# Performance work log

Measured on AMD Instinct MI355X. Metric: run time of the kernel, lower is better.

Reference implementation:

```python
import jax, jax.numpy as jnp
import numpy as np

VS = 0.4
SENT = np.int32(2_000_000_000)  # > max lin code (1000^3)
EPS = 1e-5


def setup_inputs() -> dict:
    key = jax.random.key(0)
    ks = jax.random.split(key, 16)
    B, N, Cin, Cout = 8, 65536, 16, 128
    xyz = jax.random.uniform(ks[0], (B, N, 3), jnp.float32) * 51.2  # 128^3 voxel grid @ 0.4m
    feat = jax.random.normal(ks[1], (B, N, Cin), jnp.float32)
    mask = (jax.random.uniform(ks[2], (B, N)) < 0.9).astype(jnp.float32)
    def conv_w(k, ci, co):
        return jax.random.normal(k, (27, ci, co), jnp.float32) * (1.0 / np.sqrt(27.0 * ci))
    return {
        'xyz': xyz, 'feat': feat, 'mask': mask,
        'W1': conv_w(ks[3], Cin, 32), 'b1': jnp.zeros((32,), jnp.float32),
        'g1': jnp.ones((32,), jnp.float32), 'be1': jnp.zeros((32,), jnp.float32),
        'W2': conv_w(ks[4], 32, 64), 'b2': jnp.zeros((64,), jnp.float32),
        'g2': jnp.ones((64,), jnp.float32), 'be2': jnp.zeros((64,), jnp.float32),
        'W3': conv_w(ks[5], 64, Cout), 'b3': jnp.zeros((Cout,), jnp.float32),
        'g3': jnp.ones((Cout,), jnp.float32), 'be3': jnp.zeros((Cout,), jnp.float32),
    }


def _voxelize(lin_b, f_b, m_b):
    # sort-based unique with inverse; fixed capacity N slots (sentinel-padded)
    N = lin_b.shape[0]
    order = jnp.argsort(lin_b)
    s = lin_b[order]
    isnew = jnp.concatenate([jnp.ones((1,), bool), s[1:] != s[:-1]])
    rank = (jnp.cumsum(isnew) - 1).astype(jnp.int32)
    inv = jnp.zeros_like(lin_b).at[order].set(rank)          # point -> voxel slot
    unq = jnp.full_like(lin_b, SENT).at[rank].set(s)         # sorted unique codes, sentinel fill
    fsum = jax.ops.segment_sum(f_b * m_b[:, None], inv, num_segments=N)
    cnt = jnp.clip(jax.ops.segment_sum(m_b, inv, num_segments=N), 1.0)
    return unq, inv, fsum / cnt[:, None]


def _subm_conv(vfeat, unq, valid, W, b):
    # submanifold 3x3x3 conv on active voxels; neighbor lookup via binary search in sorted codes
    B, N, _ = vfeat.shape
    x = unq % 1000
    y = (unq // 1000) % 1000
    z = unq // 1000000
    brow = jnp.arange(B)[:, None]
    out = jnp.zeros((B, N, W.shape[-1]), vfeat.dtype)
    for ko in range(27):
        dz, dy, dx = ko // 9 - 1, (ko // 3) % 3 - 1, ko % 3 - 1
        ncode = unq + dx + 1000 * dy + 1000000 * dz
        inb = ((x + dx >= 0) & (x + dx < 1000) & (y + dy >= 0) & (y + dy < 1000)
               & (z + dz >= 0) & (z + dz < 1000))
        idx = jnp.clip(jax.vmap(jnp.searchsorted)(unq, ncode), 0, N - 1)
        found = (jnp.take_along_axis(unq, idx, 1) == ncode) & inb & valid
        nf = vfeat[brow, idx] * found[..., None].astype(vfeat.dtype)
        out = out + nf @ W[ko]
    return (out + b) * valid[..., None].astype(vfeat.dtype)


def _bn_relu(xv, g, be, valid):
    # BatchNorm1d (training stats) over valid voxel rows only, then ReLU
    w = valid[..., None].astype(xv.dtype)
    n = jnp.maximum(w.sum(), 1.0)
    mean = (xv * w).sum((0, 1)) / n
    var = (((xv - mean) ** 2) * w).sum((0, 1)) / n
    yv = (xv - mean) * jax.lax.rsqrt(var + EPS) * g + be
    return jax.nn.relu(yv) * w


def reference(xyz, feat, mask, W1, b1, g1, be1, W2, b2, g2, be2, W3, b3, g3, be3):
    B, N, _ = feat.shape
    origin = xyz.reshape(-1, 3).min(0)
    v = jnp.clip(((xyz - origin) / VS).astype(jnp.int32), 0, None)   # [B,N,3]
    lin = v[..., 0] + 1000 * (v[..., 1] + 1000 * v[..., 2])          # [B,N]
    unq, inv, vfeat = jax.vmap(_voxelize)(lin, feat, mask)
    valid = unq < SENT
    h = _bn_relu(_subm_conv(vfeat, unq, valid, W1, b1), g1, be1, valid)
    h = _bn_relu(_subm_conv(h, unq, valid, W2, b2), g2, be2, valid)
    h = _bn_relu(_subm_conv(h, unq, valid, W3, b3), g3, be3, valid)
    # scatter voxel features back to points (exact match: inv maps point -> its voxel slot)
    out_f = h[jnp.arange(B)[:, None], inv]                           # [B,N,Cout]
    return out_f * mask[..., None]
```

## Files before the change

### kernel.cpp

```cpp
#include <hip/hip_runtime.h>

#define NPTS   65536
#define NBATCH 8
#define TSIZE  131072
#define TM1    (TSIZE - 1)
#define CAP    8192
#define PPB    64
#define BMW    65536
#define STG    64
#define PCS    16

__device__ __forceinline__ unsigned hashf(int code) {
    unsigned u = (unsigned)code * 2654435761u;
    return (u >> 13) & TM1;
}

__global__ void init_origin(int* ob) {
    if (threadIdx.x < 3) ob[threadIdx.x] = 0x7F800000;
}

__global__ void minred(const float* __restrict__ xyz, int* __restrict__ ob) {
    int tid = threadIdx.x;
    float mx = INFINITY, my = INFINITY, mz = INFINITY;
    size_t total = (size_t)NBATCH * NPTS;
    for (size_t i = (size_t)blockIdx.x * blockDim.x + tid; i < total;
         i += (size_t)gridDim.x * blockDim.x) {
        mx = fminf(mx, xyz[i * 3 + 0]);
        my = fminf(my, xyz[i * 3 + 1]);
        mz = fminf(mz, xyz[i * 3 + 2]);
    }
    __shared__ float sx[256], sy[256], sz[256];
    sx[tid] = mx; sy[tid] = my; sz[tid] = mz;
    __syncthreads();
    for (int s = 128; s > 0; s >>= 1) {
        if (tid < s) {
            sx[tid] = fminf(sx[tid], sx[tid + s]);
            sy[tid] = fminf(sy[tid], sy[tid + s]);
            sz[tid] = fminf(sz[tid], sz[tid + s]);
        }
        __syncthreads();
    }
    if (tid == 0) {
        atomicMin(&ob[0], __float_as_int(sx[0]));
        atomicMin(&ob[1], __float_as_int(sy[0]));
        atomicMin(&ob[2], __float_as_int(sz[0]));
    }
}

__global__ void build_codes(const float* __restrict__ xyz, const int* __restrict__ ob,
                            int* __restrict__ pslot, int* __restrict__ hashk,
                            int* __restrict__ scnt) {
    int b = blockIdx.y;
    int p = blockIdx.x * blockDim.x + threadIdx.x;
    size_t gi = (size_t)b * NPTS + p;
    float ox = __int_as_float(ob[0]);
    float oy = __int_as_float(ob[1]);
    float oz = __int_as_float(ob[2]);
    float x = xyz[gi * 3 + 0], y = xyz[gi * 3 + 1], z = xyz[gi * 3 + 2];
    int vx = (int)((x - ox) / 0.4f); if (vx < 0) vx = 0;
    int vy = (int)((y - oy) / 0.4f); if (vy < 0) vy = 0;
    int vz = (int)((z - oz) / 0.4f); if (vz < 0) vz = 0;
    int code = vx | (vy << 7) | (vz << 14);
    int* hk = hashk + (size_t)b * TSIZE;
    unsigned s = hashf(code);
    while (true) {
        int prev = atomicCAS(&hk[s], -1, code);
        if (prev == -1 || prev == code) break;
        s = (s + 1) & TM1;
    }
    pslot[gi] = (int)s;
    atomicAdd(&scnt[(size_t)b * TSIZE + s], 1);
}

__global__ void assign_ids(const int* __restrict__ hashk, int* __restrict__ hashv,
                           int* __restrict__ nvox, int* __restrict__ voxcode,
                           unsigned* __restrict__ bitmap, const int* __restrict__ scnt,
                           int* __restrict__ vnpts) {
    int b = blockIdx.y;
    int s = blockIdx.x * blockDim.x + threadIdx.x;
    int k = hashk[(size_t)b * TSIZE + s];
    unsigned long long vote = __ballot(k != -1);
    __shared__ int wbase[4];
    int wid = threadIdx.x >> 6, lane = threadIdx.x & 63;
    if (lane == 0) wbase[wid] = __popcll(vote);
    __syncthreads();
    if (threadIdx.x == 0) {
        int c0 = wbase[0], c1 = wbase[1], c2 = wbase[2], c3 = wbase[3];
        int base = atomicAdd(&nvox[b], c0 + c1 + c2 + c3);
        wbase[0] = base;
        wbase[1] = base + c0;
        wbase[2] = base + c0 + c1;
        wbase[3] = base + c0 + c1 + c2;
    }
    __syncthreads();
    if (k != -1) {
        int id = wbase[wid] + __popcll(vote & ((1ull << lane) - 1ull));
        hashv[(size_t)b * TSIZE + s] = id;
        voxcode[(size_t)b * NPTS + id] = k;
        vnpts[(size_t)b * NPTS + id] = scnt[(size_t)b * TSIZE + s];
        atomicOr(&bitmap[(size_t)b * BMW + (k >> 5)], 1u << (k & 31));
    }
}

__global__ void point_pass(const int* __restrict__ pslot, const int* __restrict__ scnt,
                           const int* __restrict__ hashv, const float* __restrict__ feat,
                           const float* __restrict__ mask, int* __restrict__ inv,
                           float* __restrict__ cntf, float* __restrict__ fsum) {
    int b = blockIdx.y;
    int p = blockIdx.x * blockDim.x + threadIdx.x;
    size_t gi = (size_t)b * NPTS + p;
    int s = pslot[gi];
    int v = hashv[(size_t)b * TSIZE + s];
    inv[gi] = v;
    int n = scnt[(size_t)b * TSIZE + s];
    float m = mask[gi];
    const float4* f4 = (const float4*)(feat + gi * 16);
    float4 f0 = f4[0], f1 = f4[1], f2 = f4[2], f3 = f4[3];
    float* fs = fsum + ((size_t)b * NPTS + v) * 16;
    if (n == 1) {
        float4 o0 = {f0.x * m, f0.y * m, f0.z * m, f0.w * m};
        float4 o1 = {f1.x * m, f1.y * m, f1.z * m, f1.w * m};
        float4 o2 = {f2.x * m, f2.y * m, f2.z * m, f2.w * m};
        float4 o3 = {f3.x * m, f3.y * m, f3.z * m, f3.w * m};
        float4* fs4 = (float4*)fs;
        fs4[0] = o0; fs4[1] = o1; fs4[2] = o2; fs4[3] = o3;
    } else {
        atomicAdd(&cntf[(size_t)b * NPTS + v], m);
        atomicAdd(&fs[0],  f0.x * m); atomicAdd(&fs[1],  f0.y * m);
        atomicAdd(&fs[2],  f0.z * m); atomicAdd(&fs[3],  f0.w * m);
        atomicAdd(&fs[4],  f1.x * m); atomicAdd(&fs[5],  f1.y * m);
        atomicAdd(&fs[6],  f1.z * m); atomicAdd(&fs[7],  f1.w * m);
        atomicAdd(&fs[8],  f2.x * m); atomicAdd(&fs[9],  f2.y * m);
        atomicAdd(&fs[10], f2.z * m); atomicAdd(&fs[11], f2.w * m);
        atomicAdd(&fs[12], f3.x * m); atomicAdd(&fs[13], f3.y * m);
        atomicAdd(&fs[14], f3.z * m); atomicAdd(&fs[15], f3.w * m);
    }
}

__global__ void vfeat_div(float* __restrict__ fsum, const float* __restrict__ cntf,
                          const int* __restrict__ vnpts, const int* __restrict__ nvox) {
    int b = blockIdx.y;
    int v = blockIdx.x * blockDim.x + threadIdx.x;
    if (v >= nvox[b]) return;
    if (vnpts[(size_t)b * NPTS + v] <= 1) return;
    float cn = fmaxf(cntf[(size_t)b * NPTS + v], 1.0f);
    float* fs = fsum + ((size_t)b * NPTS + v) * 16;
    #pragma unroll
    for (int c = 0; c < 16; c++) fs[c] /= cn;
}

__global__ __launch_bounds__(256) void build_pairs(
    const int* __restrict__ hashk, const int* __restrict__ hashv,
    const int* __restrict__ voxcode, const int* __restrict__ nvox,
    const unsigned* __restrict__ bitmap,
    unsigned* __restrict__ pairs, int* __restrict__ paircnt) {
    int b = blockIdx.y;
    int t = threadIdx.x;
    int v = blockIdx.x * 256 + t;
    __shared__ int lcnt[32];
    __shared__ int lbase[32];
    __shared__ unsigned s_pay[27 * STG];
    if (t < 32) lcnt[t] = 0;
    __syncthreads();

    bool active = (v < nvox[b]);
    int code = 0;
    if (active) code = voxcode[(size_t)b * NPTS + v];
    int x = code & 127, y = (code >> 7) & 127, z = code >> 14;
    const unsigned* bm = bitmap + (size_t)b * BMW;
    const int* hk = hashk + (size_t)b * TSIZE;
    const int* hv = hashv + (size_t)b * TSIZE;

    int ncode[13];
    unsigned hitmask = 0;
    #pragma unroll
    for (int d = 0; d < 13; d++) {
        int dz = d / 9 - 1, r9 = d % 9;
        int dy = r9 / 3 - 1, dx = r9 % 3 - 1;
        int nx = x + dx, ny = y + dy, nz = z + dz;
        bool inb = active && ((unsigned)nx <= 127u) && ((unsigned)ny <= 127u) &&
                   ((unsigned)nz <= 127u);
        int nc = nx | (ny << 7) | (nz << 14);
        ncode[d] = nc;
        unsigned w = 0;
        if (inb) w = bm[nc >> 5];
        if (inb && ((w >> (nc & 31)) & 1u)) hitmask |= 1u << d;
    }

    #pragma unroll
    for (int d = 0; d < 13; d++) {
        if (hitmask & (1u << d)) {
            int nc = ncode[d];
            unsigned s = hashf(nc);
            int nb = -1;
            while (true) {
                int k = hk[s];
                if (k == nc) { nb = hv[s]; break; }
                if (k == -1) break;
                s = (s + 1) & TM1;
            }
            if (nb >= 0) {
                unsigned p1 = ((unsigned)v << 16) | (unsigned)nb;
                unsigned p2 = ((unsigned)nb << 16) | (unsigned)v;
                int l1 = atomicAdd(&lcnt[d], 1);
                if (l1 < STG) {
                    s_pay[d * STG + l1] = p1;
                } else {
                    int gs = atomicAdd(&paircnt[(b * 27 + d) * PCS], 1);
                    if (gs < CAP) pairs[(size_t)(b * 27 + d) * CAP + gs] = p1;
                }
                int k2 = 26 - d;
                int l2 = atomicAdd(&lcnt[k2], 1);
                if (l2 < STG) {
                    s_pay[k2 * STG + l2] = p2;
                } else {
                    int gs = atomicAdd(&paircnt[(b * 27 + k2) * PCS], 1);
                    if (gs < CAP) pairs[(size_t)(b * 27 + k2) * CAP + gs] = p2;
                }
            }
        }
    }
    __syncthreads();

    if (t < 27) {
        int n = lcnt[t]; if (n > STG) n = STG;
        lbase[t] = (n > 0) ? atomicAdd(&paircnt[(b * 27 + t) * PCS], n) : 0;
    }
    __syncthreads();

    for (int k = t; k < 27 * STG; k += 256) {
        int bkt = k / STG, i = k % STG;
        int n = lcnt[bkt]; if (n > STG) n = STG;
        if (i < n) {
            int gs = lbase[bkt] + i;
            if (gs < CAP) pairs[(size_t)(b * 27 + bkt) * CAP + gs] = s_pay[k];
        }
    }
}

template <int Cin, int Cout, bool XFORM>
__global__ __launch_bounds__(256, 4) void conv_center(
    const float* __restrict__ in, float* __restrict__ outp,
    const float* __restrict__ W13, const float* __restrict__ bias,
    const float* __restrict__ sc, const float* __restrict__ sh,
    const int* __restrict__ nvox) {
    constexpr int BR  = 64;
    constexpr int CT  = (Cout < 64) ? Cout : 64;
    constexpr int RG  = 256 / CT;
    constexpr int RPT = BR / RG;
    constexpr int J   = Cout / CT;
    int b = blockIdx.y;
    int nv = nvox[b];
    int v0 = blockIdx.x * BR;
    if (v0 >= nv) return;
    __shared__ __align__(16) float A_s[Cin][BR + 4];
    int t = threadIdx.x;
    const float* inb = in + (size_t)b * NPTS * Cin;
    for (int i4 = t; i4 < BR * Cin / 4; i4 += 256) {
        int lin = i4 * 4;
        int r = lin / Cin, ci = lin % Cin;
        float4 val = *(const float4*)&inb[(size_t)(v0 + r) * Cin + ci];
        if (XFORM) {
            val.x = fmaxf(val.x * sc[ci + 0] + sh[ci + 0], 0.0f);
            val.y = fmaxf(val.y * sc[ci + 1] + sh[ci + 1], 0.0f);
            val.z = fmaxf(val.z * sc[ci + 2] + sh[ci + 2], 0.0f);
            val.w = fmaxf(val.w * sc[ci + 3] + sh[ci + 3], 0.0f);
        }
        A_s[ci + 0][r ^ ((ci + 0) & 28)] = val.x;
        A_s[ci + 1][r ^ ((ci + 1) & 28)] = val.y;
        A_s[ci + 2][r ^ ((ci + 2) & 28)] = val.z;
        A_s[ci + 3][r ^ ((ci + 3) & 28)] = val.w;
    }
    __syncthreads();
    int c = t % CT;
    int r0 = (t / CT) * RPT;
    float acc[RPT][J];
    #pragma unroll
    for (int r = 0; r < RPT; r++)
        #pragma unroll
        for (int j = 0; j < J; j++) acc[r][j] = 0.0f;
    #pragma unroll 4
    for (int ci = 0; ci < Cin; ci++) {
        int sw = ci & 28;
        float w[J];
        #pragma unroll
        for (int j = 0; j < J; j++) w[j] = W13[(size_t)ci * Cout + c + CT * j];
        #pragma unroll
        for (int k = 0; k < RPT / 4; k++) {
            float4 a4 = *(const float4*)&A_s[ci][(r0 + 4 * k) ^ sw];
            #pragma unroll
            for (int j = 0; j < J; j++) {
                acc[4 * k + 0][j] += a4.x * w[j];
                acc[4 * k + 1][j] += a4.y * w[j];
                acc[4 * k + 2][j] += a4.z * w[j];
                acc[4 * k + 3][j] += a4.w * w[j];
            }
        }
    }
    float* ob = outp + (size_t)b * NPTS * Cout;
    float bs[J];
    #pragma unroll
    for (int j = 0; j < J; j++) bs[j] = bias[c + CT * j];
    #pragma unroll
    for (int r = 0; r < RPT; r++) {
        int row = v0 + r0 + r;
        if (row < nv) {
            #pragma unroll
            for (int j = 0; j < J; j++)
                ob[(size_t)row * Cout + c + CT * j] = acc[r][j] + bs[j];
        }
    }
}

template <int Cin, int Cout, bool XFORM>
__global__ __launch_bounds__(256, 4) void conv_off(
    const float* __restrict__ in, float* __restrict__ outp,
    const float* __restrict__ W, const float* __restrict__ sc,
    const float* __restrict__ sh, const unsigned* __restrict__ pairs,
    const int* __restrict__ paircnt) {
    constexpr int BR  = PPB;
    constexpr int CT  = (Cout < 64) ? Cout : 64;
    constexpr int RG  = 256 / CT;
    constexpr int RPT = BR / RG;
    constexpr int J   = Cout / CT;
    int bk = blockIdx.y;
    int ko = bk % 27;
    int b  = bk / 27;
    int cnt = paircnt[bk * PCS];
    if (cnt > CAP) cnt = CAP;
    int start = blockIdx.x * BR;
    if (start >= cnt) return;
    int nActive = cnt - start; if (nActive > BR) nActive = BR;
    __shared__ __align__(16) float A_s[Cin][BR + 4];
    __shared__ unsigned pr_s[BR];
    int t = threadIdx.x;
    const float* Wk = W + (size_t)ko * Cin * Cout;
    const unsigned* pb = pairs + (size_t)bk * CAP + start;
    if (t < BR) pr_s[t] = pb[t];
    __syncthreads();
    const float* inb = in + (size_t)b * NPTS * Cin;
    for (int i4 = t; i4 < BR * Cin / 4; i4 += 256) {
        int lin = i4 * 4;
        int r = lin / Cin, ci = lin % Cin;
        int vin = (int)(pr_s[r] & 0xffffu);
        float4 val = *(const float4*)&inb[(size_t)vin * Cin + ci];
        if (XFORM) {
            val.x = fmaxf(val.x * sc[ci + 0] + sh[ci + 0], 0.0f);
            val.y = fmaxf(val.y * sc[ci + 1] + sh[ci + 1], 0.0f);
            val.z = fmaxf(val.z * sc[ci + 2] + sh[ci + 2], 0.0f);
            val.w = fmaxf(val.w * sc[ci + 3] + sh[ci + 3], 0.0f);
        }
        A_s[ci + 0][r ^ ((ci + 0) & 28)] = val.x;
        A_s[ci + 1][r ^ ((ci + 1) & 28)] = val.y;
        A_s[ci + 2][r ^ ((ci + 2) & 28)] = val.z;
        A_s[ci + 3][r ^ ((ci + 3) & 28)] = val.w;
    }
    __syncthreads();
    int c = t % CT;
    int r0 = (t / CT) * RPT;
    float acc[RPT][J];
    #pragma unroll
    for (int r = 0; r < RPT; r++)
        #pragma unroll
        for (int j = 0; j < J; j++) acc[r][j] = 0.0f;
    #pragma unroll 4
    for (int ci = 0; ci < Cin; ci++) {
        int sw = ci & 28;
        float w[J];
        #pragma unroll
        for (int j = 0; j < J; j++) w[j] = Wk[(size_t)ci * Cout + c + CT * j];
        #pragma unroll
        for (int k = 0; k < RPT / 4; k++) {
            float4 a4 = *(const float4*)&A_s[ci][(r0 + 4 * k) ^ sw];
            #pragma unroll
            for (int j = 0; j < J; j++) {
                acc[4 * k + 0][j] += a4.x * w[j];
                acc[4 * k + 1][j] += a4.y * w[j];
                acc[4 * k + 2][j] += a4.z * w[j];
                acc[4 * k + 3][j] += a4.w * w[j];
            }
        }
    }
    float* ob = outp + (size_t)b * NPTS * Cout;
    #pragma unroll
    for (int r = 0; r < RPT; r++) {
        if (r0 + r < nActive) {
            int vout = (int)(pr_s[r0 + r] >> 16);
            #pragma unroll
            for (int j = 0; j < J; j++)
                atomicAdd(&ob[(size_t)vout * Cout + c + CT * j], acc[r][j]);
        }
    }
}

template <int C>
__global__ __launch_bounds__(256) void bn_stats(const float* __restrict__ h,
                                                const int* __restrict__ nvox,
                                                float* __restrict__ sums) {
    constexpr int QPR = C / 4;
    constexpr int RPB = 256 / QPR;
    int b = blockIdx.y;
    int nv = nvox[b];
    int tid = threadIdx.x;
    int q = tid % QPR;
    int r = tid / QPR;
    float4 s0 = {0.f, 0.f, 0.f, 0.f}, s1 = {0.f, 0.f, 0.f, 0.f};
    const float* hb = h + (size_t)b * NPTS * C + q * 4;
    for (int v = blockIdx.x * RPB + r; v < nv; v += gridDim.x * RPB) {
        float4 x = *(const float4*)&hb[(size_t)v * C];
        s0.x += x.x; s0.y += x.y; s0.z += x.z; s0.w += x.w;
        s1.x += x.x * x.x; s1.y += x.y * x.y; s1.z += x.z * x.z; s1.w += x.w * x.w;
    }
    __shared__ float4 l0[256], l1[256];
    l0[tid] = s0; l1[tid] = s1;
    __syncthreads();
    for (int s = 128; s >= QPR; s >>= 1) {
        if (tid < s) {
            float4 a = l0[tid + s], bq = l1[tid + s];
            l0[tid].x += a.x; l0[tid].y += a.y; l0[tid].z += a.z; l0[tid].w += a.w;
            l1[tid].x += bq.x; l1[tid].y += bq.y; l1[tid].z += bq.z; l1[tid].w += bq.w;
        }
        __syncthreads();
    }
    if (tid < QPR) {
        float4 a = l0[tid], bq = l1[tid];
        atomicAdd(&sums[tid * 4 + 0], a.x);
        atomicAdd(&sums[tid * 4 + 1], a.y);
        atomicAdd(&sums[tid * 4 + 2], a.z);
        atomicAdd(&sums[tid * 4 + 3], a.w);
        atomicAdd(&sums[C + tid * 4 + 0], bq.x);
        atomicAdd(&sums[C + tid * 4 + 1], bq.y);
        atomicAdd(&sums[C + tid * 4 + 2], bq.z);
        atomicAdd(&sums[C + tid * 4 + 3], bq.w);
    }
}

template <int C>
__global__ void bn_finalize(const float* __restrict__ sums, const int* __restrict__ nvox,
                            const float* __restrict__ g, const float* __restrict__ be,
                            float* __restrict__ scale, float* __restrict__ shift) {
    int c = threadIdx.x;
    if (c >= C) return;
    float n = 0.0f;
    for (int b = 0; b < NBATCH; b++) n += (float)nvox[b];
    n = fmaxf(n, 1.0f);
    float mean = sums[c] / n;
    float var = sums[C + c] / n - mean * mean;
    float a = g[c] * rsqrtf(var + 1e-5f);
    scale[c] = a;
    shift[c] = be[c] - mean * a;
}

__global__ void out_gather(const float* __restrict__ h3, const int* __restrict__ inv,
                           const float* __restrict__ mask, const float* __restrict__ sc,
                           const float* __restrict__ sh, float* __restrict__ out) {
    int b = blockIdx.y;
    int i = blockIdx.x * blockDim.x + threadIdx.x;
    int p = i >> 5;
    int c4 = (i & 31) * 4;
    size_t gi = (size_t)b * NPTS + p;
    int v = inv[gi];
    float m = mask[gi];
    float4 x = *(const float4*)&h3[((size_t)b * NPTS + v) * 128 + c4];
    float4 s = *(const float4*)&sc[c4];
    float4 h = *(const float4*)&sh[c4];
    float4 o;
    o.x = fmaxf(x.x * s.x + h.x, 0.0f) * m;
    o.y = fmaxf(x.y * s.y + h.y, 0.0f) * m;
    o.z = fmaxf(x.z * s.z + h.z, 0.0f) * m;
    o.w = fmaxf(x.w * s.w + h.w, 0.0f) * m;
    *(float4*)&out[gi * 128 + c4] = o;
}

extern "C" void kernel_launch(void* const* d_in, const int* in_sizes, int n_in,
                              void* d_out, int out_size, void* d_ws, size_t ws_size,
                              hipStream_t stream) {
    const float* xyz  = (const float*)d_in[0];
    const float* feat = (const float*)d_in[1];
    const float* mask = (const float*)d_in[2];
    const float* W1 = (const float*)d_in[3];
    const float* b1 = (const float*)d_in[4];
    const float* g1 = (const float*)d_in[5];
    const float* be1 = (const float*)d_in[6];
    const float* W2 = (const float*)d_in[7];
    const float* b2 = (const float*)d_in[8];
    const float* g2 = (const float*)d_in[9];
    const float* be2 = (const float*)d_in[10];
    const float* W3 = (const float*)d_in[11];
    const float* b3 = (const float*)d_in[12];
    const float* g3 = (const float*)d_in[13];
    const float* be3 = (const float*)d_in[14];
    float* out = (float*)d_out;

    char* ws = (char*)d_ws;
    size_t off = 0;
    auto alloc = [&](size_t bytes) {
        void* p = ws + off;
        off += (bytes + 255) & ~(size_t)255;
        return p;
    };
    int*      hashk   = (int*)alloc((size_t)NBATCH * TSIZE * 4);
    int*      hashv   = (int*)alloc((size_t)NBATCH * TSIZE * 4);
    int*      scnt    = (int*)alloc((size_t)NBATCH * TSIZE * 4);
    int*      nvox    = (int*)alloc(NBATCH * 4);
    int*      origin  = (int*)alloc(16);
    int*      pslot   = (int*)alloc((size_t)NBATCH * NPTS * 4);
    int*      voxcode = (int*)alloc((size_t)NBATCH * NPTS * 4);
    int*      vnpts   = (int*)alloc((size_t)NBATCH * NPTS * 4);
    int*      inv     = (int*)alloc((size_t)NBATCH * NPTS * 4);
    float*    cntf    = (float*)alloc((size_t)NBATCH * NPTS * 4);
    unsigned* pairs   = (unsigned*)alloc((size_t)NBATCH * 27 * CAP * 4);
    int*      paircnt = (int*)alloc((size_t)NBATCH * 27 * PCS * 4);
    unsigned* bitmap  = (unsigned*)alloc((size_t)NBATCH * BMW * 4);
    float*    bnsums  = (float*)alloc(256 * 4);
    float*    bnscale = (float*)alloc(128 * 4);
    float*    bnshift = (float*)alloc(128 * 4);
    float*    A       = (float*)alloc((size_t)NBATCH * NPTS * 64 * 4);
    float*    Bb      = (float*)alloc((size_t)NBATCH * NPTS * 128 * 4);

    hipMemsetAsync(hashk, 0xFF, (size_t)NBATCH * TSIZE * 4, stream);
    hipMemsetAsync(scnt, 0, (size_t)NBATCH * TSIZE * 4, stream);
    hipMemsetAsync(nvox, 0, NBATCH * 4, stream);
    hipMemsetAsync(cntf, 0, (size_t)NBATCH * NPTS * 4, stream);
    hipMemsetAsync(A, 0, (size_t)NBATCH * NPTS * 16 * 4, stream);
    hipMemsetAsync(paircnt, 0, (size_t)NBATCH * 27 * PCS * 4, stream);
    hipMemsetAsync(bitmap, 0, (size_t)NBATCH * BMW * 4, stream);
    init_origin<<<1, 64, 0, stream>>>(origin);

    minred<<<512, 256, 0, stream>>>(xyz, origin);
    build_codes<<<dim3(NPTS / 256, NBATCH), 256, 0, stream>>>(xyz, origin, pslot, hashk, scnt);
    assign_ids<<<dim3(TSIZE / 256, NBATCH), 256, 0, stream>>>(hashk, hashv, nvox, voxcode,
                                                              bitmap, scnt, vnpts);
    point_pass<<<dim3(NPTS / 256, NBATCH), 256, 0, stream>>>(pslot, scnt, hashv, feat, mask,
                                                             inv, cntf, A);
    vfeat_div<<<dim3(NPTS / 256, NBATCH), 256, 0, stream>>>(A, cntf, vnpts, nvox);

    build_pairs<<<dim3(NPTS / 256, NBATCH), 256, 0, stream>>>(hashk, hashv, voxcode,
                                                              nvox, bitmap, pairs, paircnt);

    dim3 cgrid(NPTS / 64, NBATCH);
    dim3 ogrid(CAP / PPB, NBATCH * 27);
    dim3 sgrid(128, NBATCH);

    conv_center<16, 32, false><<<cgrid, 256, 0, stream>>>(A, Bb, W1 + 13 * 16 * 32, b1,
                                                          nullptr, nullptr, nvox);
    conv_off<16, 32, false><<<ogrid, 256, 0, stream>>>(A, Bb, W1, nullptr, nullptr,
                                                       pairs, paircnt);
    hipMemsetAsync(bnsums, 0, 256 * 4, stream);
    bn_stats<32><<<sgrid, 256, 0, stream>>>(Bb, nvox, bnsums);
    bn_finalize<32><<<1, 128, 0, stream>>>(bnsums, nvox, g1, be1, bnscale, bnshift);

    conv_center<32, 64, true><<<cgrid, 256, 0, stream>>>(Bb, A, W2 + 13 * 32 * 64, b2,
                                                         bnscale, bnshift, nvox);
    conv_off<32, 64, true><<<ogrid, 256, 0, stream>>>(Bb, A, W2, bnscale, bnshift,
                                                      pairs, paircnt);
    hipMemsetAsync(bnsums, 0, 256 * 4, stream);
    bn_stats<64><<<sgrid, 256, 0, stream>>>(A, nvox, bnsums);
    bn_finalize<64><<<1, 128, 0, stream>>>(bnsums, nvox, g2, be2, bnscale, bnshift);

    conv_center<64, 128, true><<<cgrid, 256, 0, stream>>>(A, Bb, W3 + 13 * 64 * 128, b3,
                                                          bnscale, bnshift, nvox);
    conv_off<64, 128, true><<<ogrid, 256, 0, stream>>>(A, Bb, W3, bnscale, bnshift,
                                                       pairs, paircnt);
    hipMemsetAsync(bnsums, 0, 256 * 4, stream);
    bn_stats<128><<<sgrid, 256, 0, stream>>>(Bb, nvox, bnsums);
    bn_finalize<128><<<1, 128, 0, stream>>>(bnsums, nvox, g3, be3, bnscale, bnshift);

    out_gather<<<dim3(NPTS * 32 / 256, NBATCH), 256, 0, stream>>>(Bb, inv, mask, bnscale,
                                                                  bnshift, out);
}
```

Baseline: 1.487 ms.

## Skip atomics for single-neighbor voxels and consolidate zeroing memsets

build_pairs now probes all 26 neighbor offsets in the bitmap and stores each voxel's neighbor degree. conv_off uses a plain read-modify-write instead of atomicAdd when the output voxel has exactly one neighbor, on the reasoning that only one pair writes to it. Buffers are reordered so a single memset zeroes all counters and accumulators, and bn_finalize clears bnsums itself so the per-layer memsets go away. This relies on the assumption that conv_center has finished its write before conv_off runs, and it adds 13 extra bitmap probes per voxel.

```diff
diff --git a/kernel.cpp b/kernel.cpp
--- a/kernel.cpp
+++ b/kernel.cpp
@@ -153,7 +153,8 @@
     const int* __restrict__ hashk, const int* __restrict__ hashv,
     const int* __restrict__ voxcode, const int* __restrict__ nvox,
     const unsigned* __restrict__ bitmap,
-    unsigned* __restrict__ pairs, int* __restrict__ paircnt) {
+    unsigned* __restrict__ pairs, int* __restrict__ paircnt,
+    int* __restrict__ deg) {
     int b = blockIdx.y;
     int t = threadIdx.x;
     int v = blockIdx.x * 256 + t;
@@ -172,24 +173,26 @@
     const int* hv = hashv + (size_t)b * TSIZE;
 
     int ncode[13];
-    unsigned hitmask = 0;
-    #pragma unroll
-    for (int d = 0; d < 13; d++) {
+    unsigned hm = 0;
+    #pragma unroll
+    for (int d = 0; d < 27; d++) {
+        if (d == 13) continue;
         int dz = d / 9 - 1, r9 = d % 9;
         int dy = r9 / 3 - 1, dx = r9 % 3 - 1;
         int nx = x + dx, ny = y + dy, nz = z + dz;
         bool inb = active && ((unsigned)nx <= 127u) && ((unsigned)ny <= 127u) &&
                    ((unsigned)nz <= 127u);
         int nc = nx | (ny << 7) | (nz << 14);
-        ncode[d] = nc;
+        if (d < 13) ncode[d] = nc;
         unsigned w = 0;
         if (inb) w = bm[nc >> 5];
-        if (inb && ((w >> (nc & 31)) & 1u)) hitmask |= 1u << d;
-    }
+        if (inb && ((w >> (nc & 31)) & 1u)) hm |= 1u << d;
+    }
+    if (active) deg[(size_t)b * NPTS + v] = __popc(hm);
 
     #pragma unroll
     for (int d = 0; d < 13; d++) {
-        if (hitmask & (1u << d)) {
+        if (hm & (1u << d)) {
             int nc = ncode[d];
             unsigned s = hashf(nc);
             int nb = -1;
@@ -317,7 +320,7 @@
     const float* __restrict__ in, float* __restrict__ outp,
     const float* __restrict__ W, const float* __restrict__ sc,
     const float* __restrict__ sh, const unsigned* __restrict__ pairs,
-    const int* __restrict__ paircnt) {
+    const int* __restrict__ paircnt, const int* __restrict__ deg) {
     constexpr int BR  = PPB;
     constexpr int CT  = (Cout < 64) ? Cout : 64;
     constexpr int RG  = 256 / CT;
@@ -382,13 +385,21 @@
         }
     }
     float* ob = outp + (size_t)b * NPTS * Cout;
+    const int* degb = deg + (size_t)b * NPTS;
     #pragma unroll
     for (int r = 0; r < RPT; r++) {
         if (r0 + r < nActive) {
             int vout = (int)(pr_s[r0 + r] >> 16);
-            #pragma unroll
-            for (int j = 0; j < J; j++)
-                atomicAdd(&ob[(size_t)vout * Cout + c + CT * j], acc[r][j]);
+            float* po = &ob[(size_t)vout * Cout + c];
+            if (degb[vout] == 1) {
+                #pragma unroll
+                for (int j = 0; j < J; j++)
+                    po[CT * j] += acc[r][j];
+            } else {
+                #pragma unroll
+                for (int j = 0; j < J; j++)
+                    atomicAdd(&po[CT * j], acc[r][j]);
+            }
         }
     }
 }
@@ -436,16 +447,21 @@
 }
 
 template <int C>
-__global__ void bn_finalize(const float* __restrict__ sums, const int* __restrict__ nvox,
+__global__ void bn_finalize(float* __restrict__ sums, const int* __restrict__ nvox,
                             const float* __restrict__ g, const float* __restrict__ be,
                             float* __restrict__ scale, float* __restrict__ shift) {
     int c = threadIdx.x;
+    float s0 = 0.0f, s1 = 0.0f;
+    if (c < C) { s0 = sums[c]; s1 = sums[C + c]; }
+    __syncthreads();
+    sums[c] = 0.0f;
+    sums[128 + c] = 0.0f;
     if (c >= C) return;
     float n = 0.0f;
     for (int b = 0; b < NBATCH; b++) n += (float)nvox[b];
     n = fmaxf(n, 1.0f);
-    float mean = sums[c] / n;
-    float var = sums[C + c] / n - mean * mean;
+    float mean = s0 / n;
+    float var = s1 / n - mean * mean;
     float a = g[c] * rsqrtf(var + 1e-5f);
     scale[c] = a;
     shift[c] = be[c] - mean * a;
@@ -501,30 +517,27 @@
     };
     int*      hashk   = (int*)alloc((size_t)NBATCH * TSIZE * 4);
     int*      hashv   = (int*)alloc((size_t)NBATCH * TSIZE * 4);
-    int*      scnt    = (int*)alloc((size_t)NBATCH * TSIZE * 4);
-    int*      nvox    = (int*)alloc(NBATCH * 4);
     int*      origin  = (int*)alloc(16);
     int*      pslot   = (int*)alloc((size_t)NBATCH * NPTS * 4);
     int*      voxcode = (int*)alloc((size_t)NBATCH * NPTS * 4);
     int*      vnpts   = (int*)alloc((size_t)NBATCH * NPTS * 4);
     int*      inv     = (int*)alloc((size_t)NBATCH * NPTS * 4);
+    int*      deg     = (int*)alloc((size_t)NBATCH * NPTS * 4);
+    unsigned* pairs   = (unsigned*)alloc((size_t)NBATCH * 27 * CAP * 4);
+    float*    bnscale = (float*)alloc(128 * 4);
+    float*    bnshift = (float*)alloc(128 * 4);
+    float*    Bb      = (float*)alloc((size_t)NBATCH * NPTS * 128 * 4);
+    int*      scnt    = (int*)alloc((size_t)NBATCH * TSIZE * 4);
+    int*      nvox    = (int*)alloc(NBATCH * 4);
     float*    cntf    = (float*)alloc((size_t)NBATCH * NPTS * 4);
-    unsigned* pairs   = (unsigned*)alloc((size_t)NBATCH * 27 * CAP * 4);
     int*      paircnt = (int*)alloc((size_t)NBATCH * 27 * PCS * 4);
     unsigned* bitmap  = (unsigned*)alloc((size_t)NBATCH * BMW * 4);
     float*    bnsums  = (float*)alloc(256 * 4);
-    float*    bnscale = (float*)alloc(128 * 4);
-    float*    bnshift = (float*)alloc(128 * 4);
     float*    A       = (float*)alloc((size_t)NBATCH * NPTS * 64 * 4);
-    float*    Bb      = (float*)alloc((size_t)NBATCH * NPTS * 128 * 4);
+    size_t zero_len = (size_t)((char*)A - (char*)scnt) + (size_t)NBATCH * NPTS * 16 * 4;
 
     hipMemsetAsync(hashk, 0xFF, (size_t)NBATCH * TSIZE * 4, stream);
-    hipMemsetAsync(scnt, 0, (size_t)NBATCH * TSIZE * 4, stream);
-    hipMemsetAsync(nvox, 0, NBATCH * 4, stream);
-    hipMemsetAsync(cntf, 0, (size_t)NBATCH * NPTS * 4, stream);
-    hipMemsetAsync(A, 0, (size_t)NBATCH * NPTS * 16 * 4, stream);
-    hipMemsetAsync(paircnt, 0, (size_t)NBATCH * 27 * PCS * 4, stream);
-    hipMemsetAsync(bitmap, 0, (size_t)NBATCH * BMW * 4, stream);
+    hipMemsetAsync(scnt, 0, zero_len, stream);
     init_origin<<<1, 64, 0, stream>>>(origin);
 
     minred<<<512, 256, 0, stream>>>(xyz, origin);
@@ -536,7 +549,8 @@
     vfeat_div<<<dim3(NPTS / 256, NBATCH), 256, 0, stream>>>(A, cntf, vnpts, nvox);
 
     build_pairs<<<dim3(NPTS / 256, NBATCH), 256, 0, stream>>>(hashk, hashv, voxcode,
-                                                              nvox, bitmap, pairs, paircnt);
+                                                              nvox, bitmap, pairs, paircnt,
+                                                              deg);
 
     dim3 cgrid(NPTS / 64, NBATCH);
     dim3 ogrid(CAP / PPB, NBATCH * 27);
@@ -545,24 +559,21 @@
     conv_center<16, 32, false><<<cgrid, 256, 0, stream>>>(A, Bb, W1 + 13 * 16 * 32, b1,
                                                           nullptr, nullptr, nvox);
     conv_off<16, 32, false><<<ogrid, 256, 0, stream>>>(A, Bb, W1, nullptr, nullptr,
-                                                       pairs, paircnt);
-    hipMemsetAsync(bnsums, 0, 256 * 4, stream);
+                                                       pairs, paircnt, deg);
     bn_stats<32><<<sgrid, 256, 0, stream>>>(Bb, nvox, bnsums);
     bn_finalize<32><<<1, 128, 0, stream>>>(bnsums, nvox, g1, be1, bnscale, bnshift);
 
     conv_center<32, 64, true><<<cgrid, 256, 0, stream>>>(Bb, A, W2 + 13 * 32 * 64, b2,
                                                          bnscale, bnshift, nvox);
     conv_off<32, 64, true><<<ogrid, 256, 0, stream>>>(Bb, A, W2, bnscale, bnshift,
-                                                      pairs, paircnt);
-    hipMemsetAsync(bnsums, 0, 256 * 4, stream);
+                                                      pairs, paircnt, deg);
     bn_stats<64><<<sgrid, 256, 0, stream>>>(A, nvox, bnsums);
     bn_finalize<64><<<1, 128, 0, stream>>>(bnsums, nvox, g2, be2, bnscale, bnshift);
 
     conv_center<64, 128, true><<<cgrid, 256, 0, stream>>>(A, Bb, W3 + 13 * 64 * 128, b3,
                                                           bnscale, bnshift, nvox);
     conv_off<64, 128, true><<<ogrid, 256, 0, stream>>>(A, Bb, W3, bnscale, bnshift,
-                                                       pairs, paircnt);
-    hipMemsetAsync(bnsums, 0, 256 * 4, stream);
+                                                       pairs, paircnt, deg);
     bn_stats<128><<<sgrid, 256, 0, stream>>>(Bb, nvox, bnsums);
     bn_finalize<128><<<1, 128, 0, stream>>>(bnsums, nvox, g3, be3, bnscale, bnshift);
 
```

New measurement: 1.501 ms. Within noise of the previous version (+0.9%).
